# Optimization experiments

Measured on AMD Instinct MI355X. Metric: run time of the kernel, lower is better.

Reference implementation:

```python
import jax, jax.numpy as jnp
import numpy as np

B, N, E = 4, 256, 512  # batch, max_sentence_len, embedding_size


def setup_inputs() -> dict:
    key = jax.random.key(0)
    k1, k2, k3 = jax.random.split(key, 3)
    inputs = jax.random.normal(k1, (B, N, E), dtype=jnp.float32)
    scale = 1.0 / np.sqrt(N)
    queries_weight = jax.random.normal(k2, (N, N), dtype=jnp.float32) * scale
    keys_weight = jax.random.normal(k3, (N, N), dtype=jnp.float32) * scale
    return {"inputs": inputs, "queries_weight": queries_weight, "keys_weight": keys_weight}


def reference(inputs, queries_weight, keys_weight):
    # Original math: for each position i, weights are masked to the top-left
    # (i+1)x(i+1) block:  QW[i,n,p] = Qw[n,p]*(n<=i)*(p<=i)  (same for keys).
    # queries[b,i,m,p] = sum_{n<=i} x[b,n,m] Qw[n,p] * (p<=i)  -> cumsum over n.
    # keys[b,i,p,q]    = sum_{n<=i} x[b,n,q] Kw[n,p] * (p<=i)
    # attn[b,i,m,q] = sum_p queries[b,i,m,p] keys[b,i,p,q]
    # fit[b,i,m]    = sum_q attn[b,i,m,q] x[b,i,q]
    #               = sum_p queries[b,i,m,p] * (sum_q keys[b,i,p,q] x[b,i,q])
    # The (p<=i) mask appears squared, so applying it once suffices.
    b, n, e = inputs.shape
    tri = jnp.tril(jnp.ones((n, n), dtype=inputs.dtype))  # tri[i,p] = (p <= i)

    # (B,N,E,N): cumulative (over source position) outer products
    Qcum = jnp.cumsum(jnp.einsum('bnm,np->bnmp', inputs, queries_weight), axis=1)
    Qcum = Qcum * tri[None, :, None, :]
    Kcum = jnp.cumsum(jnp.einsum('bnq,np->bnqp', inputs, keys_weight), axis=1)

    s = jnp.einsum('biqp,biq->bip', Kcum, inputs)      # keys contracted with x_i
    fitnesses = jnp.einsum('bimp,bip->bim', Qcum, s)   # (B,N,E)
    avg_fitness = jnp.einsum('bim,bim->bi', inputs, fitnesses)[..., None]
    net_fitnesses = fitnesses - avg_fitness
    return inputs + inputs * net_fitnesses
```

## Files before the change

kernel.cpp:

```cpp
#include <hip/hip_runtime.h>

#define B_ 4
#define N_ 256
#define E_ 512

#define OFF_GP 65536
#define OFF_SP 1114112
#define OFF_TP 2162688

__global__ __launch_bounds__(256) void prep_kernel(
    const float* __restrict__ X, const float* __restrict__ Qw,
    float* __restrict__ QwT, float* __restrict__ Gpart) {

    const int bx = blockIdx.x, by = blockIdx.y, bz = blockIdx.z;
    const int tx = threadIdx.x, ty = threadIdx.y;
    const int tid = ty * 16 + tx;

    if (bz == 16) {
        __shared__ float tt[64][68];
        const int r = tid >> 2, c0 = tid & 3;
#pragma unroll
        for (int cc = 0; cc < 4; ++cc) {
            const int c = (c0 + cc * 4) * 4;
            const float4 v = *(const float4*)&Qw[(by * 64 + r) * N_ + bx * 64 + c];
            tt[c + 0][r] = v.x; tt[c + 1][r] = v.y;
            tt[c + 2][r] = v.z; tt[c + 3][r] = v.w;
        }
        __syncthreads();
#pragma unroll
        for (int cc = 0; cc < 4; ++cc) {
            const int c = (c0 + cc * 4) * 4;
            const float4 v = *(const float4*)&tt[r][c];
            *(float4*)&QwT[(bx * 64 + r) * N_ + by * 64 + c] = v;
        }
        return;
    }

    const int b = bz >> 2, kq = bz & 3;
    const float* __restrict__ Xb = X + (size_t)b * N_ * E_;
    __shared__ float At[32][68];
    __shared__ float Bt[32][68];
    float acc[4][4] = {};
    const int r = tid >> 2, c0 = tid & 3;

    for (int k0 = kq * 128; k0 < kq * 128 + 128; k0 += 32) {
        {
            const float4 va = *(const float4*)&Xb[(size_t)(by * 64 + r) * E_ + k0 + c0 * 8];
            const float4 vb = *(const float4*)&Xb[(size_t)(by * 64 + r) * E_ + k0 + c0 * 8 + 4];
            At[c0*8+0][r] = va.x; At[c0*8+1][r] = va.y; At[c0*8+2][r] = va.z; At[c0*8+3][r] = va.w;
            At[c0*8+4][r] = vb.x; At[c0*8+5][r] = vb.y; At[c0*8+6][r] = vb.z; At[c0*8+7][r] = vb.w;
            const float4 wa = *(const float4*)&Xb[(size_t)(bx * 64 + r) * E_ + k0 + c0 * 8];
            const float4 wb = *(const float4*)&Xb[(size_t)(bx * 64 + r) * E_ + k0 + c0 * 8 + 4];
            Bt[c0*8+0][r] = wa.x; Bt[c0*8+1][r] = wa.y; Bt[c0*8+2][r] = wa.z; Bt[c0*8+3][r] = wa.w;
            Bt[c0*8+4][r] = wb.x; Bt[c0*8+5][r] = wb.y; Bt[c0*8+6][r] = wb.z; Bt[c0*8+7][r] = wb.w;
        }
        __syncthreads();
#pragma unroll
        for (int kk = 0; kk < 32; ++kk) {
            const float4 a  = *(const float4*)&At[kk][ty * 4];
            const float4 bb = *(const float4*)&Bt[kk][tx * 4];
            acc[0][0] += a.x*bb.x; acc[0][1] += a.x*bb.y; acc[0][2] += a.x*bb.z; acc[0][3] += a.x*bb.w;
            acc[1][0] += a.y*bb.x; acc[1][1] += a.y*bb.y; acc[1][2] += a.y*bb.z; acc[1][3] += a.y*bb.w;
            acc[2][0] += a.z*bb.x; acc[2][1] += a.z*bb.y; acc[2][2] += a.z*bb.z; acc[2][3] += a.z*bb.w;
            acc[3][0] += a.w*bb.x; acc[3][1] += a.w*bb.y; acc[3][2] += a.w*bb.z; acc[3][3] += a.w*bb.w;
        }
        __syncthreads();
    }
    float* gout = Gpart + ((size_t)(kq * 4 + b) * N_ + by * 64 + ty * 4) * N_ + bx * 64 + tx * 4;
#pragma unroll
    for (int qi = 0; qi < 4; ++qi)
        *(float4*)&gout[(size_t)qi * N_] =
            make_float4(acc[qi][0], acc[qi][1], acc[qi][2], acc[qi][3]);
}

__global__ __launch_bounds__(256) void sgemm_kernel(
    const float* __restrict__ Kw, float* __restrict__ ws) {

    const int pt = blockIdx.x, it = blockIdx.y;
    const int b  = blockIdx.z >> 2, kq = blockIdx.z & 3;
    if (pt > it || kq > it) return;

    const float* __restrict__ Gpart = ws + OFF_GP;
    float* __restrict__ Spart = ws + OFF_SP;

    const int tx = threadIdx.x, ty = threadIdx.y;
    const int tid = ty * 16 + tx;

    __shared__ float At[64][68];
    __shared__ float Bt[64][68];

    {
        const int i_loc = tid >> 2, c0 = tid & 3;
        float av[16];
#pragma unroll
        for (int e = 0; e < 16; ++e) av[e] = 0.f;
#pragma unroll
        for (int q = 0; q < 4; ++q) {
            const float* src = Gpart + ((size_t)(q * 4 + b) * N_ + it * 64 + i_loc) * N_
                             + kq * 64 + c0 * 16;
#pragma unroll
            for (int v = 0; v < 4; ++v) {
                const float4 f = *(const float4*)&src[v * 4];
                av[v*4+0] += f.x; av[v*4+1] += f.y; av[v*4+2] += f.z; av[v*4+3] += f.w;
            }
        }
        if (kq == it) {
#pragma unroll
            for (int e = 0; e < 16; ++e)
                if (c0 * 16 + e > i_loc) av[e] = 0.f;
        }
#pragma unroll
        for (int e = 0; e < 16; ++e) At[c0 * 16 + e][i_loc] = av[e];
    }
    {
        const int k = tid >> 2, c0 = tid & 3;
        const float* src = Kw + (size_t)(kq * 64 + k) * N_ + pt * 64 + c0 * 16;
#pragma unroll
        for (int v = 0; v < 4; ++v)
            *(float4*)&Bt[k][c0 * 16 + v * 4] = *(const float4*)&src[v * 4];
    }
    __syncthreads();

    float acc[4][4] = {};
#pragma unroll 8
    for (int kk = 0; kk < 64; ++kk) {
        const float4 a  = *(const float4*)&At[kk][ty * 4];
        const float4 bb = *(const float4*)&Bt[kk][tx * 4];
        acc[0][0] += a.x*bb.x; acc[0][1] += a.x*bb.y; acc[0][2] += a.x*bb.z; acc[0][3] += a.x*bb.w;
        acc[1][0] += a.y*bb.x; acc[1][1] += a.y*bb.y; acc[1][2] += a.y*bb.z; acc[1][3] += a.y*bb.w;
        acc[2][0] += a.z*bb.x; acc[2][1] += a.z*bb.y; acc[2][2] += a.z*bb.z; acc[2][3] += a.z*bb.w;
        acc[3][0] += a.w*bb.x; acc[3][1] += a.w*bb.y; acc[3][2] += a.w*bb.z; acc[3][3] += a.w*bb.w;
    }

    float* sout = Spart + ((size_t)(kq * 4 + b) * N_ + it * 64 + ty * 4) * N_ + pt * 64 + tx * 4;
#pragma unroll
    for (int ri = 0; ri < 4; ++ri)
        *(float4*)&sout[(size_t)ri * N_] =
            make_float4(acc[ri][0], acc[ri][1], acc[ri][2], acc[ri][3]);
}

__global__ __launch_bounds__(256) void tgemm_kernel(
    const float* __restrict__ ws_c, float* __restrict__ ws) {

    const int nt = blockIdx.x, it = blockIdx.y;
    const int b  = blockIdx.z >> 2, kp = blockIdx.z & 3;
    if (nt > it || kp > it) return;

    const float* __restrict__ QwT   = ws_c;
    const float* __restrict__ Spart = ws_c + OFF_SP;
    float* __restrict__ Tpart = ws + OFF_TP;

    const int tx = threadIdx.x, ty = threadIdx.y;
    const int tid = ty * 16 + tx;

    __shared__ float At[64][68];
    __shared__ float Bt[64][68];

    {
        const int i_loc = tid >> 2, c0 = tid & 3;
        float av[16];
#pragma unroll
        for (int e = 0; e < 16; ++e) av[e] = 0.f;
        for (int q = 0; q <= it; ++q) {
            const float* src = Spart + ((size_t)(q * 4 + b) * N_ + it * 64 + i_loc) * N_
                             + kp * 64 + c0 * 16;
#pragma unroll
            for (int v = 0; v < 4; ++v) {
                const float4 f = *(const float4*)&src[v * 4];
                av[v*4+0] += f.x; av[v*4+1] += f.y; av[v*4+2] += f.z; av[v*4+3] += f.w;
            }
        }
        if (kp == it) {
#pragma unroll
            for (int e = 0; e < 16; ++e)
                if (c0 * 16 + e > i_loc) av[e] = 0.f;
        }
#pragma unroll
        for (int e = 0; e < 16; ++e) At[c0 * 16 + e][i_loc] = av[e];
    }
    {
        const int k = tid >> 2, c0 = tid & 3;
        const float* src = QwT + (size_t)(kp * 64 + k) * N_ + nt * 64 + c0 * 16;
#pragma unroll
        for (int v = 0; v < 4; ++v)
            *(float4*)&Bt[k][c0 * 16 + v * 4] = *(const float4*)&src[v * 4];
    }
    __syncthreads();

    float acc[4][4] = {};
#pragma unroll 8
    for (int kk = 0; kk < 64; ++kk) {
        const float4 a  = *(const float4*)&At[kk][ty * 4];
        const float4 bb = *(const float4*)&Bt[kk][tx * 4];
        acc[0][0] += a.x*bb.x; acc[0][1] += a.x*bb.y; acc[0][2] += a.x*bb.z; acc[0][3] += a.x*bb.w;
        acc[1][0] += a.y*bb.x; acc[1][1] += a.y*bb.y; acc[1][2] += a.y*bb.z; acc[1][3] += a.y*bb.w;
        acc[2][0] += a.z*bb.x; acc[2][1] += a.z*bb.y; acc[2][2] += a.z*bb.z; acc[2][3] += a.z*bb.w;
        acc[3][0] += a.w*bb.x; acc[3][1] += a.w*bb.y; acc[3][2] += a.w*bb.z; acc[3][3] += a.w*bb.w;
    }

    float* tout = Tpart + ((size_t)(kp * 4 + b) * N_ + it * 64 + ty * 4) * N_ + nt * 64 + tx * 4;
#pragma unroll
    for (int ri = 0; ri < 4; ++ri)
        *(float4*)&tout[(size_t)ri * N_] =
            make_float4(acc[ri][0], acc[ri][1], acc[ri][2], acc[ri][3]);
}

__global__ __launch_bounds__(256) void final_kernel(
    const float* __restrict__ X, const float* __restrict__ ws_c,
    float* __restrict__ out) {

    const int mt = blockIdx.x, rt = blockIdx.y, b = blockIdx.z;
    const int it_eff = rt >> 1;
    const int ibase  = (rt & 1) * 32;

    const float* __restrict__ Gpart = ws_c + OFF_GP;
    const float* __restrict__ Tpart = ws_c + OFF_TP;
    const float* __restrict__ Xb = X + (size_t)b * N_ * E_;

    const int tx = threadIdx.x, ty = threadIdx.y;
    const int tid = ty * 16 + tx;

    __shared__ float At[64][36];
    __shared__ float Bt[64][68];
    __shared__ float avr[32][9];

    float acc[2][4] = {};
    float avgacc = 0.f;

    for (int kn = 0; kn <= it_eff; ++kn) {
        {
            const int r = tid >> 3, c0 = tid & 7;
            float tvv[8], gvv[8];
#pragma unroll
            for (int e = 0; e < 8; ++e) { tvv[e] = 0.f; gvv[e] = 0.f; }
            for (int q = 0; q <= it_eff; ++q) {
                const float* src = Tpart + ((size_t)(q * 4 + b) * N_ + rt * 32 + r) * N_
                                 + kn * 64 + c0 * 8;
#pragma unroll
                for (int v = 0; v < 2; ++v) {
                    const float4 f = *(const float4*)&src[v * 4];
                    tvv[v*4+0] += f.x; tvv[v*4+1] += f.y; tvv[v*4+2] += f.z; tvv[v*4+3] += f.w;
                }
            }
#pragma unroll
            for (int q = 0; q < 4; ++q) {
                const float* src = Gpart + ((size_t)(q * 4 + b) * N_ + rt * 32 + r) * N_
                                 + kn * 64 + c0 * 8;
#pragma unroll
                for (int v = 0; v < 2; ++v) {
                    const float4 f = *(const float4*)&src[v * 4];
                    gvv[v*4+0] += f.x; gvv[v*4+1] += f.y; gvv[v*4+2] += f.z; gvv[v*4+3] += f.w;
                }
            }
            if (kn == it_eff) {
#pragma unroll
                for (int e = 0; e < 8; ++e)
                    if (c0 * 8 + e > ibase + r) tvv[e] = 0.f;
            }
#pragma unroll
            for (int e = 0; e < 8; ++e) {
                avgacc += tvv[e] * gvv[e];
                At[c0 * 8 + e][r] = tvv[e];
            }
        }
        {
            const int k = tid >> 2, c0 = tid & 3;
            const float* src = Xb + (size_t)(kn * 64 + k) * E_ + mt * 64 + c0 * 16;
#pragma unroll
            for (int v = 0; v < 4; ++v)
                *(float4*)&Bt[k][c0 * 16 + v * 4] = *(const float4*)&src[v * 4];
        }
        __syncthreads();

#pragma unroll 8
        for (int kk = 0; kk < 64; ++kk) {
            const float2 a  = *(const float2*)&At[kk][ty * 2];
            const float4 bb = *(const float4*)&Bt[kk][tx * 4];
            acc[0][0] += a.x*bb.x; acc[0][1] += a.x*bb.y; acc[0][2] += a.x*bb.z; acc[0][3] += a.x*bb.w;
            acc[1][0] += a.y*bb.x; acc[1][1] += a.y*bb.y; acc[1][2] += a.y*bb.z; acc[1][3] += a.y*bb.w;
        }
        __syncthreads();
    }

    avr[tid >> 3][tid & 7] = avgacc;
    __syncthreads();

#pragma unroll
    for (int ri = 0; ri < 2; ++ri) {
        const int row = ty * 2 + ri;
        float avg = 0.f;
#pragma unroll
        for (int c = 0; c < 8; ++c) avg += avr[row][c];
        const int gi = rt * 32 + row;
        const float4 xv = *(const float4*)&Xb[(size_t)gi * E_ + mt * 64 + tx * 4];
        float4 ov;
        ov.x = xv.x * (1.f + acc[ri][0] - avg);
        ov.y = xv.y * (1.f + acc[ri][1] - avg);
        ov.z = xv.z * (1.f + acc[ri][2] - avg);
        ov.w = xv.w * (1.f + acc[ri][3] - avg);
        *(float4*)&out[((size_t)b * N_ + gi) * E_ + mt * 64 + tx * 4] = ov;
    }
}

extern "C" void kernel_launch(void* const* d_in, const int* in_sizes, int n_in,
                              void* d_out, int out_size, void* d_ws, size_t ws_size,
                              hipStream_t stream) {
    const float* X  = (const float*)d_in[0];
    const float* Qw = (const float*)d_in[1];
    const float* Kw = (const float*)d_in[2];
    float* out = (float*)d_out;
    float* ws  = (float*)d_ws;

    float* QwT   = ws;
    float* Gpart = ws + OFF_GP;

    prep_kernel <<<dim3(4, 4, 17), dim3(16, 16), 0, stream>>>(X, Qw, QwT, Gpart);
    sgemm_kernel<<<dim3(4, 4, 16), dim3(16, 16), 0, stream>>>(Kw, ws);
    tgemm_kernel<<<dim3(4, 4, 16), dim3(16, 16), 0, stream>>>(ws, ws);
    final_kernel<<<dim3(8, 8, 4),  dim3(16, 16), 0, stream>>>(X, ws, out);
}
```

Baseline: 100.5 us.

## Merge four kernels into one cooperative persistent kernel with grid syncs

Replaces the four separate launches (prep, sgemm, tgemm, final) with one cooperative kernel of 272 blocks that runs each stage in turn, separated by grid.sync(). It also compacts the triangular sgemm/tgemm work into 120 active blocks through explicit index tables instead of launching a full grid where most blocks exit early. The goal is to remove per-launch overhead and the drain/fill gaps between kernels. In exchange it adds grid-wide barrier cost, needs all 272 blocks to be co-resident, and leaves many blocks idle during the middle stages.

Measured after the change: 206.5 us. 106% more time.

```diff
diff --git a/kernel.cpp b/kernel.cpp
--- a/kernel.cpp
+++ b/kernel.cpp
@@ -1,4 +1,7 @@
 #include <hip/hip_runtime.h>
+#include <hip/hip_cooperative_groups.h>
+
+namespace cg = cooperative_groups;
 
 #define B_ 4
 #define N_ 256
@@ -8,297 +11,297 @@
 #define OFF_SP 1114112
 #define OFF_TP 2162688
 
-__global__ __launch_bounds__(256) void prep_kernel(
+__global__ __launch_bounds__(256, 4) void mono_kernel(
     const float* __restrict__ X, const float* __restrict__ Qw,
-    float* __restrict__ QwT, float* __restrict__ Gpart) {
-
-    const int bx = blockIdx.x, by = blockIdx.y, bz = blockIdx.z;
+    const float* __restrict__ Kw, float* __restrict__ ws,
+    float* __restrict__ out) {
+
+    cg::grid_group grid = cg::this_grid();
+
+    __shared__ float lds[2 * 64 * 68];
+    float* const At = lds;
+    float* const Bt = lds + 64 * 68;
+
+    const int blk = blockIdx.x;
     const int tx = threadIdx.x, ty = threadIdx.y;
     const int tid = ty * 16 + tx;
 
-    if (bz == 16) {
-        __shared__ float tt[64][68];
+    float* const QwT   = ws;
+    float* const Gpart = ws + OFF_GP;
+    float* const Spart = ws + OFF_SP;
+    float* const Tpart = ws + OFF_TP;
+
+    if (blk < 256) {
+        const int kq = blk >> 6;
+        const int rem = blk & 63;
+        const int b = rem >> 4;
+        const int tileid = rem & 15;
+        const int by = tileid >> 2, bx = tileid & 3;
+        const float* __restrict__ Xb = X + (size_t)b * N_ * E_;
+        float acc[4][4] = {};
+        const int r = tid >> 2, c0 = tid & 3;
+
+        for (int k0 = kq * 128; k0 < kq * 128 + 128; k0 += 32) {
+            {
+                const float4 va = *(const float4*)&Xb[(size_t)(by * 64 + r) * E_ + k0 + c0 * 8];
+                const float4 vb = *(const float4*)&Xb[(size_t)(by * 64 + r) * E_ + k0 + c0 * 8 + 4];
+                At[(c0*8+0)*68+r] = va.x; At[(c0*8+1)*68+r] = va.y;
+                At[(c0*8+2)*68+r] = va.z; At[(c0*8+3)*68+r] = va.w;
+                At[(c0*8+4)*68+r] = vb.x; At[(c0*8+5)*68+r] = vb.y;
+                At[(c0*8+6)*68+r] = vb.z; At[(c0*8+7)*68+r] = vb.w;
+                const float4 wa = *(const float4*)&Xb[(size_t)(bx * 64 + r) * E_ + k0 + c0 * 8];
+                const float4 wb = *(const float4*)&Xb[(size_t)(bx * 64 + r) * E_ + k0 + c0 * 8 + 4];
+                Bt[(c0*8+0)*68+r] = wa.x; Bt[(c0*8+1)*68+r] = wa.y;
+                Bt[(c0*8+2)*68+r] = wa.z; Bt[(c0*8+3)*68+r] = wa.w;
+                Bt[(c0*8+4)*68+r] = wb.x; Bt[(c0*8+5)*68+r] = wb.y;
+                Bt[(c0*8+6)*68+r] = wb.z; Bt[(c0*8+7)*68+r] = wb.w;
+            }
+            __syncthreads();
+#pragma unroll
+            for (int kk = 0; kk < 32; ++kk) {
+                const float4 a  = *(const float4*)&At[kk * 68 + ty * 4];
+                const float4 bb = *(const float4*)&Bt[kk * 68 + tx * 4];
+                acc[0][0] += a.x*bb.x; acc[0][1] += a.x*bb.y; acc[0][2] += a.x*bb.z; acc[0][3] += a.x*bb.w;
+                acc[1][0] += a.y*bb.x; acc[1][1] += a.y*bb.y; acc[1][2] += a.y*bb.z; acc[1][3] += a.y*bb.w;
+                acc[2][0] += a.z*bb.x; acc[2][1] += a.z*bb.y; acc[2][2] += a.z*bb.z; acc[2][3] += a.z*bb.w;
+                acc[3][0] += a.w*bb.x; acc[3][1] += a.w*bb.y; acc[3][2] += a.w*bb.z; acc[3][3] += a.w*bb.w;
+            }
+            __syncthreads();
+        }
+        float* gout = Gpart + ((size_t)(kq * 4 + b) * N_ + by * 64 + ty * 4) * N_ + bx * 64 + tx * 4;
+#pragma unroll
+        for (int ri = 0; ri < 4; ++ri)
+            *(float4*)&gout[(size_t)ri * N_] =
+                make_float4(acc[ri][0], acc[ri][1], acc[ri][2], acc[ri][3]);
+    } else {
+        const int t = blk - 256;
+        const int bxt = t & 3, byt = t >> 2;
         const int r = tid >> 2, c0 = tid & 3;
 #pragma unroll
         for (int cc = 0; cc < 4; ++cc) {
             const int c = (c0 + cc * 4) * 4;
-            const float4 v = *(const float4*)&Qw[(by * 64 + r) * N_ + bx * 64 + c];
-            tt[c + 0][r] = v.x; tt[c + 1][r] = v.y;
-            tt[c + 2][r] = v.z; tt[c + 3][r] = v.w;
+            const float4 v = *(const float4*)&Qw[(byt * 64 + r) * N_ + bxt * 64 + c];
+            At[(c+0)*68+r] = v.x; At[(c+1)*68+r] = v.y;
+            At[(c+2)*68+r] = v.z; At[(c+3)*68+r] = v.w;
         }
         __syncthreads();
 #pragma unroll
         for (int cc = 0; cc < 4; ++cc) {
             const int c = (c0 + cc * 4) * 4;
-            const float4 v = *(const float4*)&tt[r][c];
-            *(float4*)&QwT[(bx * 64 + r) * N_ + by * 64 + c] = v;
-        }
-        return;
+            const float4 v = *(const float4*)&At[r * 68 + c];
+            *(float4*)&QwT[(bxt * 64 + r) * N_ + byt * 64 + c] = v;
+        }
     }
 
-    const int b = bz >> 2, kq = bz & 3;
-    const float* __restrict__ Xb = X + (size_t)b * N_ * E_;
-    __shared__ float At[32][68];
-    __shared__ float Bt[32][68];
-    float acc[4][4] = {};
-    const int r = tid >> 2, c0 = tid & 3;
-
-    for (int k0 = kq * 128; k0 < kq * 128 + 128; k0 += 32) {
+    grid.sync();
+
+    if (blk < 120) {
+        const int b = blk / 30;
+        const int r2 = blk % 30;
+        int it, pt, kq;
+        if (r2 < 1)       { it = 0; pt = 0;              kq = 0; }
+        else if (r2 < 5)  { it = 1; const int q = r2-1;  pt = q >> 1; kq = q & 1; }
+        else if (r2 < 14) { it = 2; const int q = r2-5;  pt = q / 3;  kq = q % 3; }
+        else              { it = 3; const int q = r2-14; pt = q >> 2; kq = q & 3; }
+
         {
-            const float4 va = *(const float4*)&Xb[(size_t)(by * 64 + r) * E_ + k0 + c0 * 8];
-            const float4 vb = *(const float4*)&Xb[(size_t)(by * 64 + r) * E_ + k0 + c0 * 8 + 4];
-            At[c0*8+0][r] = va.x; At[c0*8+1][r] = va.y; At[c0*8+2][r] = va.z; At[c0*8+3][r] = va.w;
-            At[c0*8+4][r] = vb.x; At[c0*8+5][r] = vb.y; At[c0*8+6][r] = vb.z; At[c0*8+7][r] = vb.w;
-            const float4 wa = *(const float4*)&Xb[(size_t)(bx * 64 + r) * E_ + k0 + c0 * 8];
-            const float4 wb = *(const float4*)&Xb[(size_t)(bx * 64 + r) * E_ + k0 + c0 * 8 + 4];
-            Bt[c0*8+0][r] = wa.x; Bt[c0*8+1][r] = wa.y; Bt[c0*8+2][r] = wa.z; Bt[c0*8+3][r] = wa.w;
-            Bt[c0*8+4][r] = wb.x; Bt[c0*8+5][r] = wb.y; Bt[c0*8+6][r] = wb.z; Bt[c0*8+7][r] = wb.w;
+            const int i_loc = tid >> 2, c0 = tid & 3;
+            float av[16];
+#pragma unroll
+            for (int e = 0; e < 16; ++e) av[e] = 0.f;
+#pragma unroll
+            for (int q = 0; q < 4; ++q) {
+                const float* src = Gpart + ((size_t)(q * 4 + b) * N_ + it * 64 + i_loc) * N_
+                                 + kq * 64 + c0 * 16;
+#pragma unroll
+                for (int v = 0; v < 4; ++v) {
+                    const float4 f = *(const float4*)&src[v * 4];
+                    av[v*4+0] += f.x; av[v*4+1] += f.y; av[v*4+2] += f.z; av[v*4+3] += f.w;
+                }
+            }
+            if (kq == it) {
+#pragma unroll
+                for (int e = 0; e < 16; ++e)
+                    if (c0 * 16 + e > i_loc) av[e] = 0.f;
+            }
+#pragma unroll
+            for (int e = 0; e < 16; ++e) At[(c0 * 16 + e) * 68 + i_loc] = av[e];
+        }
+        {
+            const int k = tid >> 2, c0 = tid & 3;
+            const float* src = Kw + (size_t)(kq * 64 + k) * N_ + pt * 64 + c0 * 16;
+#pragma unroll
+            for (int v = 0; v < 4; ++v)
+                *(float4*)&Bt[k * 68 + c0 * 16 + v * 4] = *(const float4*)&src[v * 4];
         }
         __syncthreads();
-#pragma unroll
-        for (int kk = 0; kk < 32; ++kk) {
-            const float4 a  = *(const float4*)&At[kk][ty * 4];
-            const float4 bb = *(const float4*)&Bt[kk][tx * 4];
+
+        float acc[4][4] = {};
+#pragma unroll 8
+        for (int kk = 0; kk < 64; ++kk) {
+            const float4 a  = *(const float4*)&At[kk * 68 + ty * 4];
+            const float4 bb = *(const float4*)&Bt[kk * 68 + tx * 4];
             acc[0][0] += a.x*bb.x; acc[0][1] += a.x*bb.y; acc[0][2] += a.x*bb.z; acc[0][3] += a.x*bb.w;
             acc[1][0] += a.y*bb.x; acc[1][1] += a.y*bb.y; acc[1][2] += a.y*bb.z; acc[1][3] += a.y*bb.w;
             acc[2][0] += a.z*bb.x; acc[2][1] += a.z*bb.y; acc[2][2] += a.z*bb.z; acc[2][3] += a.z*bb.w;
             acc[3][0] += a.w*bb.x; acc[3][1] += a.w*bb.y; acc[3][2] += a.w*bb.z; acc[3][3] += a.w*bb.w;
         }
-        __syncthreads();
+
+        float* sout = Spart + ((size_t)(kq * 4 + b) * N_ + it * 64 + ty * 4) * N_ + pt * 64 + tx * 4;
+#pragma unroll
+        for (int ri = 0; ri < 4; ++ri)
+            *(float4*)&sout[(size_t)ri * N_] =
+                make_float4(acc[ri][0], acc[ri][1], acc[ri][2], acc[ri][3]);
     }
-    float* gout = Gpart + ((size_t)(kq * 4 + b) * N_ + by * 64 + ty * 4) * N_ + bx * 64 + tx * 4;
-#pragma unroll
-    for (int qi = 0; qi < 4; ++qi)
-        *(float4*)&gout[(size_t)qi * N_] =
-            make_float4(acc[qi][0], acc[qi][1], acc[qi][2], acc[qi][3]);
-}
-
-__global__ __launch_bounds__(256) void sgemm_kernel(
-    const float* __restrict__ Kw, float* __restrict__ ws) {
-
-    const int pt = blockIdx.x, it = blockIdx.y;
-    const int b  = blockIdx.z >> 2, kq = blockIdx.z & 3;
-    if (pt > it || kq > it) return;
-
-    const float* __restrict__ Gpart = ws + OFF_GP;
-    float* __restrict__ Spart = ws + OFF_SP;
-
-    const int tx = threadIdx.x, ty = threadIdx.y;
-    const int tid = ty * 16 + tx;
-
-    __shared__ float At[64][68];
-    __shared__ float Bt[64][68];
-
-    {
-        const int i_loc = tid >> 2, c0 = tid & 3;
-        float av[16];
-#pragma unroll
-        for (int e = 0; e < 16; ++e) av[e] = 0.f;
-#pragma unroll
-        for (int q = 0; q < 4; ++q) {
-            const float* src = Gpart + ((size_t)(q * 4 + b) * N_ + it * 64 + i_loc) * N_
-                             + kq * 64 + c0 * 16;
-#pragma unroll
-            for (int v = 0; v < 4; ++v) {
-                const float4 f = *(const float4*)&src[v * 4];
-                av[v*4+0] += f.x; av[v*4+1] += f.y; av[v*4+2] += f.z; av[v*4+3] += f.w;
-            }
-        }
-        if (kq == it) {
-#pragma unroll
-            for (int e = 0; e < 16; ++e)
-                if (c0 * 16 + e > i_loc) av[e] = 0.f;
-        }
-#pragma unroll
-        for (int e = 0; e < 16; ++e) At[c0 * 16 + e][i_loc] = av[e];
-    }
-    {
-        const int k = tid >> 2, c0 = tid & 3;
-        const float* src = Kw + (size_t)(kq * 64 + k) * N_ + pt * 64 + c0 * 16;
-#pragma unroll
-        for (int v = 0; v < 4; ++v)
-            *(float4*)&Bt[k][c0 * 16 + v * 4] = *(const float4*)&src[v * 4];
-    }
-    __syncthreads();
-
-    float acc[4][4] = {};
-#pragma unroll 8
-    for (int kk = 0; kk < 64; ++kk) {
-        const float4 a  = *(const float4*)&At[kk][ty * 4];
-        const float4 bb = *(const float4*)&Bt[kk][tx * 4];
-        acc[0][0] += a.x*bb.x; acc[0][1] += a.x*bb.y; acc[0][2] += a.x*bb.z; acc[0][3] += a.x*bb.w;
-        acc[1][0] += a.y*bb.x; acc[1][1] += a.y*bb.y; acc[1][2] += a.y*bb.z; acc[1][3] += a.y*bb.w;
-        acc[2][0] += a.z*bb.x; acc[2][1] += a.z*bb.y; acc[2][2] += a.z*bb.z; acc[2][3] += a.z*bb.w;
-        acc[3][0] += a.w*bb.x; acc[3][1] += a.w*bb.y; acc[3][2] += a.w*bb.z; acc[3][3] += a.w*bb.w;
-    }
-
-    float* sout = Spart + ((size_t)(kq * 4 + b) * N_ + it * 64 + ty * 4) * N_ + pt * 64 + tx * 4;
-#pragma unroll
-    for (int ri = 0; ri < 4; ++ri)
-        *(float4*)&sout[(size_t)ri * N_] =
-            make_float4(acc[ri][0], acc[ri][1], acc[ri][2], acc[ri][3]);
-}
-
-__global__ __launch_bounds__(256) void tgemm_kernel(
-    const float* __restrict__ ws_c, float* __restrict__ ws) {
-
-    const int nt = blockIdx.x, it = blockIdx.y;
-    const int b  = blockIdx.z >> 2, kp = blockIdx.z & 3;
-    if (nt > it || kp > it) return;
-
-    const float* __restrict__ QwT   = ws_c;
-    const float* __restrict__ Spart = ws_c + OFF_SP;
-    float* __restrict__ Tpart = ws + OFF_TP;
-
-    const int tx = threadIdx.x, ty = threadIdx.y;
-    const int tid = ty * 16 + tx;
-
-    __shared__ float At[64][68];
-    __shared__ float Bt[64][68];
-
-    {
-        const int i_loc = tid >> 2, c0 = tid & 3;
-        float av[16];
-#pragma unroll
-        for (int e = 0; e < 16; ++e) av[e] = 0.f;
-        for (int q = 0; q <= it; ++q) {
-            const float* src = Spart + ((size_t)(q * 4 + b) * N_ + it * 64 + i_loc) * N_
-                             + kp * 64 + c0 * 16;
-#pragma unroll
-            for (int v = 0; v < 4; ++v) {
-                const float4 f = *(const float4*)&src[v * 4];
-                av[v*4+0] += f.x; av[v*4+1] += f.y; av[v*4+2] += f.z; av[v*4+3] += f.w;
-            }
-        }
-        if (kp == it) {
-#pragma unroll
-            for (int e = 0; e < 16; ++e)
-                if (c0 * 16 + e > i_loc) av[e] = 0.f;
-        }
-#pragma unroll
-        for (int e = 0; e < 16; ++e) At[c0 * 16 + e][i_loc] = av[e];
-    }
-    {
-        const int k = tid >> 2, c0 = tid & 3;
-        const float* src = QwT + (size_t)(kp * 64 + k) * N_ + nt * 64 + c0 * 16;
-#pragma unroll
-        for (int v = 0; v < 4; ++v)
-            *(float4*)&Bt[k][c0 * 16 + v * 4] = *(const float4*)&src[v * 4];
-    }
-    __syncthreads();
-
-    float acc[4][4] = {};
-#pragma unroll 8
-    for (int kk = 0; kk < 64; ++kk) {
-        const float4 a  = *(const float4*)&At[kk][ty * 4];
-        const float4 bb = *(const float4*)&Bt[kk][tx * 4];
-        acc[0][0] += a.x*bb.x; acc[0][1] += a.x*bb.y; acc[0][2] += a.x*bb.z; acc[0][3] += a.x*bb.w;
-        acc[1][0] += a.y*bb.x; acc[1][1] += a.y*bb.y; acc[1][2] += a.y*bb.z; acc[1][3] += a.y*bb.w;
-        acc[2][0] += a.z*bb.x; acc[2][1] += a.z*bb.y; acc[2][2] += a.z*bb.z; acc[2][3] += a.z*bb.w;
-        acc[3][0] += a.w*bb.x; acc[3][1] += a.w*bb.y; acc[3][2] += a.w*bb.z; acc[3][3] += a.w*bb.w;
-    }
-
-    float* tout = Tpart + ((size_t)(kp * 4 + b) * N_ + it * 64 + ty * 4) * N_ + nt * 64 + tx * 4;
-#pragma unroll
-    for (int ri = 0; ri < 4; ++ri)
-        *(float4*)&tout[(size_t)ri * N_] =
-            make_float4(acc[ri][0], acc[ri][1], acc[ri][2], acc[ri][3]);
-}
-
-__global__ __launch_bounds__(256) void final_kernel(
-    const float* __restrict__ X, const float* __restrict__ ws_c,
-    float* __restrict__ out) {
-
-    const int mt = blockIdx.x, rt = blockIdx.y, b = blockIdx.z;
-    const int it_eff = rt >> 1;
-    const int ibase  = (rt & 1) * 32;
-
-    const float* __restrict__ Gpart = ws_c + OFF_GP;
-    const float* __restrict__ Tpart = ws_c + OFF_TP;
-    const float* __restrict__ Xb = X + (size_t)b * N_ * E_;
-
-    const int tx = threadIdx.x, ty = threadIdx.y;
-    const int tid = ty * 16 + tx;
-
-    __shared__ float At[64][36];
-    __shared__ float Bt[64][68];
-    __shared__ float avr[32][9];
-
-    float acc[2][4] = {};
-    float avgacc = 0.f;
-
-    for (int kn = 0; kn <= it_eff; ++kn) {
+
+    grid.sync();
+
+    if (blk < 120) {
+        const int b = blk / 30;
+        const int r2 = blk % 30;
+        int it, nt, kp;
+        if (r2 < 1)       { it = 0; nt = 0;              kp = 0; }
+        else if (r2 < 5)  { it = 1; const int q = r2-1;  nt = q >> 1; kp = q & 1; }
+        else if (r2 < 14) { it = 2; const int q = r2-5;  nt = q / 3;  kp = q % 3; }
+        else              { it = 3; const int q = r2-14; nt = q >> 2; kp = q & 3; }
+
         {
-            const int r = tid >> 3, c0 = tid & 7;
-            float tvv[8], gvv[8];
-#pragma unroll
-            for (int e = 0; e < 8; ++e) { tvv[e] = 0.f; gvv[e] = 0.f; }
-            for (int q = 0; q <= it_eff; ++q) {
-                const float* src = Tpart + ((size_t)(q * 4 + b) * N_ + rt * 32 + r) * N_
-                                 + kn * 64 + c0 * 8;
-#pragma unroll
-                for (int v = 0; v < 2; ++v) {
+            const int i_loc = tid >> 2, c0 = tid & 3;
+            float av[16];
+#pragma unroll
+            for (int e = 0; e < 16; ++e) av[e] = 0.f;
+            for (int q = 0; q <= it; ++q) {
+                const float* src = Spart + ((size_t)(q * 4 + b) * N_ + it * 64 + i_loc) * N_
+                                 + kp * 64 + c0 * 16;
+#pragma unroll
+                for (int v = 0; v < 4; ++v) {
                     const float4 f = *(const float4*)&src[v * 4];
-                    tvv[v*4+0] += f.x; tvv[v*4+1] += f.y; tvv[v*4+2] += f.z; tvv[v*4+3] += f.w;
-                }
-            }
-#pragma unroll
-            for (int q = 0; q < 4; ++q) {
-                const float* src = Gpart + ((size_t)(q * 4 + b) * N_ + rt * 32 + r) * N_
-                                 + kn * 64 + c0 * 8;
-#pragma unroll
-                for (int v = 0; v < 2; ++v) {
-                    const float4 f = *(const float4*)&src[v * 4];
-                    gvv[v*4+0] += f.x; gvv[v*4+1] += f.y; gvv[v*4+2] += f.z; gvv[v*4+3] += f.w;
-                }
-            }
-            if (kn == it_eff) {
-#pragma unroll
-                for (int e = 0; e < 8; ++e)
-                    if (c0 * 8 + e > ibase + r) tvv[e] = 0.f;
-            }
-#pragma unroll
-            for (int e = 0; e < 8; ++e) {
-                avgacc += tvv[e] * gvv[e];
-                At[c0 * 8 + e][r] = tvv[e];
-            }
+                    av[v*4+0] += f.x; av[v*4+1] += f.y; av[v*4+2] += f.z; av[v*4+3] += f.w;
+                }
+            }
+            if (kp == it) {
+#pragma unroll
+                for (int e = 0; e < 16; ++e)
+                    if (c0 * 16 + e > i_loc) av[e] = 0.f;
+            }
+#pragma unroll
+            for (int e = 0; e < 16; ++e) At[(c0 * 16 + e) * 68 + i_loc] = av[e];
         }
         {
             const int k = tid >> 2, c0 = tid & 3;
-            const float* src = Xb + (size_t)(kn * 64 + k) * E_ + mt * 64 + c0 * 16;
+            const float* src = QwT + (size_t)(kp * 64 + k) * N_ + nt * 64 + c0 * 16;
 #pragma unroll
             for (int v = 0; v < 4; ++v)
-                *(float4*)&Bt[k][c0 * 16 + v * 4] = *(const float4*)&src[v * 4];
+                *(float4*)&Bt[k * 68 + c0 * 16 + v * 4] = *(const float4*)&src[v * 4];
         }
         __syncthreads();
 
+        float acc[4][4] = {};
 #pragma unroll 8
         for (int kk = 0; kk < 64; ++kk) {
-            const float2 a  = *(const float2*)&At[kk][ty * 2];
-            const float4 bb = *(const float4*)&Bt[kk][tx * 4];
+            const float4 a  = *(const float4*)&At[kk * 68 + ty * 4];
+            const float4 bb = *(const float4*)&Bt[kk * 68 + tx * 4];
             acc[0][0] += a.x*bb.x; acc[0][1] += a.x*bb.y; acc[0][2] += a.x*bb.z; acc[0][3] += a.x*bb.w;
             acc[1][0] += a.y*bb.x; acc[1][1] += a.y*bb.y; acc[1][2] += a.y*bb.z; acc[1][3] += a.y*bb.w;
-        }
+            acc[2][0] += a.z*bb.x; acc[2][1] += a.z*bb.y; acc[2][2] += a.z*bb.z; acc[2][3] += a.z*bb.w;
+            acc[3][0] += a.w*bb.x; acc[3][1] += a.w*bb.y; acc[3][2] += a.w*bb.z; acc[3][3] += a.w*bb.w;
+        }
+
+        float* tout = Tpart + ((size_t)(kp * 4 + b) * N_ + it * 64 + ty * 4) * N_ + nt * 64 + tx * 4;
+#pragma unroll
+        for (int ri = 0; ri < 4; ++ri)
+            *(float4*)&tout[(size_t)ri * N_] =
+                make_float4(acc[ri][0], acc[ri][1], acc[ri][2], acc[ri][3]);
+    }
+
+    grid.sync();
+
+    if (blk < 256) {
+        const int mt = blk & 7, rt = (blk >> 3) & 7, b = blk >> 6;
+        const int it_eff = rt >> 1;
+        const int ibase  = (rt & 1) * 32;
+        const float* __restrict__ Xb = X + (size_t)b * N_ * E_;
+
+        float* const Atf = lds;
+        float* const Btf = lds + 64 * 36;
+        float* const avr = lds + 64 * 36 + 64 * 68;
+
+        float acc[2][4] = {};
+        float avgacc = 0.f;
+
+        for (int kn = 0; kn <= it_eff; ++kn) {
+            {
+                const int r = tid >> 3, c0 = tid & 7;
+                float tvv[8], gvv[8];
+#pragma unroll
+                for (int e = 0; e < 8; ++e) { tvv[e] = 0.f; gvv[e] = 0.f; }
+                for (int q = 0; q <= it_eff; ++q) {
+                    const float* src = Tpart + ((size_t)(q * 4 + b) * N_ + rt * 32 + r) * N_
+                                     + kn * 64 + c0 * 8;
+#pragma unroll
+                    for (int v = 0; v < 2; ++v) {
+                        const float4 f = *(const float4*)&src[v * 4];
+                        tvv[v*4+0] += f.x; tvv[v*4+1] += f.y; tvv[v*4+2] += f.z; tvv[v*4+3] += f.w;
+                    }
+                }
+#pragma unroll
+                for (int q = 0; q < 4; ++q) {
+                    const float* src = Gpart + ((size_t)(q * 4 + b) * N_ + rt * 32 + r) * N_
+                                     + kn * 64 + c0 * 8;
+#pragma unroll
+                    for (int v = 0; v < 2; ++v) {
+                        const float4 f = *(const float4*)&src[v * 4];
+                        gvv[v*4+0] += f.x; gvv[v*4+1] += f.y; gvv[v*4+2] += f.z; gvv[v*4+3] += f.w;
+                    }
+                }
+                if (kn == it_eff) {
+#pragma unroll
+                    for (int e = 0; e < 8; ++e)
+                        if (c0 * 8 + e > ibase + r) tvv[e] = 0.f;
+                }
+#pragma unroll
+                for (int e = 0; e < 8; ++e) {
+                    avgacc += tvv[e] * gvv[e];
+                    Atf[(c0 * 8 + e) * 36 + r] = tvv[e];
+                }
+            }
+            {
+                const int k = tid >> 2, c0 = tid & 3;
+                const float* src = Xb + (size_t)(kn * 64 + k) * E_ + mt * 64 + c0 * 16;
+#pragma unroll
+                for (int v = 0; v < 4; ++v)
+                    *(float4*)&Btf[k * 68 + c0 * 16 + v * 4] = *(const float4*)&src[v * 4];
+            }
+            __syncthreads();
+
+#pragma unroll 8
+            for (int kk = 0; kk < 64; ++kk) {
+                const float2 a  = *(const float2*)&Atf[kk * 36 + ty * 2];
+                const float4 bb = *(const float4*)&Btf[kk * 68 + tx * 4];
+                acc[0][0] += a.x*bb.x; acc[0][1] += a.x*bb.y; acc[0][2] += a.x*bb.z; acc[0][3] += a.x*bb.w;
+                acc[1][0] += a.y*bb.x; acc[1][1] += a.y*bb.y; acc[1][2] += a.y*bb.z; acc[1][3] += a.y*bb.w;
+            }
+            __syncthreads();
+        }
+
+        avr[(tid >> 3) * 9 + (tid & 7)] = avgacc;
         __syncthreads();
-    }
-
-    avr[tid >> 3][tid & 7] = avgacc;
-    __syncthreads();
-
-#pragma unroll
-    for (int ri = 0; ri < 2; ++ri) {
-        const int row = ty * 2 + ri;
-        float avg = 0.f;
-#pragma unroll
-        for (int c = 0; c < 8; ++c) avg += avr[row][c];
-        const int gi = rt * 32 + row;
-        const float4 xv = *(const float4*)&Xb[(size_t)gi * E_ + mt * 64 + tx * 4];
-        float4 ov;
-        ov.x = xv.x * (1.f + acc[ri][0] - avg);
-        ov.y = xv.y * (1.f + acc[ri][1] - avg);
-        ov.z = xv.z * (1.f + acc[ri][2] - avg);
-        ov.w = xv.w * (1.f + acc[ri][3] - avg);
-        *(float4*)&out[((size_t)b * N_ + gi) * E_ + mt * 64 + tx * 4] = ov;
+
+#pragma unroll
+        for (int ri = 0; ri < 2; ++ri) {
+            const int row = ty * 2 + ri;
+            float avg = 0.f;
+#pragma unroll
+            for (int c = 0; c < 8; ++c) avg += avr[row * 9 + c];
+            const int gi = rt * 32 + row;
+            const float4 xv = *(const float4*)&Xb[(size_t)gi * E_ + mt * 64 + tx * 4];
+            float4 ov;
+            ov.x = xv.x * (1.f + acc[ri][0] - avg);
+            ov.y = xv.y * (1.f + acc[ri][1] - avg);
+            ov.z = xv.z * (1.f + acc[ri][2] - avg);
+            ov.w = xv.w * (1.f + acc[ri][3] - avg);
+            *(float4*)&out[((size_t)b * N_ + gi) * E_ + mt * 64 + tx * 4] = ov;
+        }
     }
 }
 
@@ -311,11 +314,7 @@
     float* out = (float*)d_out;
     float* ws  = (float*)d_ws;
 
-    float* QwT   = ws;
-    float* Gpart = ws + OFF_GP;
-
-    prep_kernel <<<dim3(4, 4, 17), dim3(16, 16), 0, stream>>>(X, Qw, QwT, Gpart);
-    sgemm_kernel<<<dim3(4, 4, 16), dim3(16, 16), 0, stream>>>(Kw, ws);
-    tgemm_kernel<<<dim3(4, 4, 16), dim3(16, 16), 0, stream>>>(ws, ws);
-    final_kernel<<<dim3(8, 8, 4),  dim3(16, 16), 0, stream>>>(X, ws, out);
+    void* args[] = { (void*)&X, (void*)&Qw, (void*)&Kw, (void*)&ws, (void*)&out };
+    hipLaunchCooperativeKernel((const void*)mono_kernel, dim3(272), dim3(16, 16),
+                               args, 0, stream);
 }
```
